# Optimization experiments

Hardware: AMD Instinct MI355X
Metric: run time of the kernel (lower is better)

Reference implementation:

```python
import jax, jax.numpy as jnp
import numpy as np


def setup_inputs() -> dict:
    key = jax.random.key(0)
    k1, k2, k3, k4 = jax.random.split(key, 4)
    dim, b, q_len, c_len = 1024, 16, 1024, 2048
    q = jax.random.normal(k1, (q_len, b, dim), dtype=jnp.float32)
    c = jax.random.normal(k2, (c_len, b, dim), dtype=jnp.float32)
    # torch nn.Linear weights: [out_features, in_features]
    W_in = jax.random.normal(k3, (dim, dim), dtype=jnp.float32) * (dim ** -0.5)
    W_out = jax.random.normal(k4, (dim, 2 * dim), dtype=jnp.float32) * ((2 * dim) ** -0.5)
    return {"q": q, "c": c, "W_in": W_in, "W_out": W_out}


def reference(q, c, W_in, W_out):
    # q: [q_len, b, dim] -> [b, q_len, dim]; c: [c_len, b, dim] -> [b, c_len, dim]
    qb = jnp.transpose(q, (1, 0, 2))
    cb = jnp.transpose(c, (1, 0, 2))
    qb = jnp.einsum('bqd,ed->bqe', qb, W_in)            # linear_in (no bias)
    score = jnp.einsum('bqd,bkd->bqk', qb, cb)          # unscaled QK^T
    score = jax.nn.softmax(score, axis=-1)              # [b, q_len, c_len]
    ctx = jnp.einsum('bqk,bkd->bqd', score, cb)         # score @ c
    cat = jnp.concatenate([ctx, qb], axis=-1)           # [b, q_len, 2*dim]
    out = jnp.tanh(jnp.einsum('bqf,df->bqd', cat, W_out))
    return (jnp.transpose(out, (1, 0, 2)), score)       # ([q_len,b,dim], [b,q_len,c_len])
```

## Files before the change

### kernel.cpp

```cpp
#include <hip/hip_runtime.h>
#include <hip/hip_bf16.h>
#include <stdint.h>


typedef __bf16 bf16x8 __attribute__((ext_vector_type(8)));
typedef float floatx4 __attribute__((ext_vector_type(4)));

__device__ __forceinline__ unsigned short f2bf_rne(float f) {
  unsigned int u = __float_as_uint(f);
  u += 0x7FFFu + ((u >> 16) & 1u);
  return (unsigned short)(u >> 16);
}
__device__ __forceinline__ float bf2f(unsigned short h) {
  return __uint_as_float(((unsigned int)h) << 16);
}

__device__ __forceinline__ void async_load16(const void* g, void* l) {
  __builtin_amdgcn_global_load_lds(
      (const __attribute__((address_space(1))) void*)g,
      (__attribute__((address_space(3))) void*)l,
      16, 0, 0);
}

__global__ __launch_bounds__(256) void split_kernel(
    const float* __restrict__ x, unsigned short* __restrict__ hi,
    unsigned short* __restrict__ lo, long n4)
{
  long i = (long)blockIdx.x * 256 + threadIdx.x;
  if (i >= n4) return;
  float4 v = ((const float4*)x)[i];
  ushort4 h;
  h.x = f2bf_rne(v.x); h.y = f2bf_rne(v.y);
  h.z = f2bf_rne(v.z); h.w = f2bf_rne(v.w);
  ((ushort4*)hi)[i] = h;
  if (lo) {
    ushort4 l;
    l.x = f2bf_rne(v.x - bf2f(h.x));
    l.y = f2bf_rne(v.y - bf2f(h.y));
    l.z = f2bf_rne(v.z - bf2f(h.z));
    l.w = f2bf_rne(v.w - bf2f(h.w));
    ((ushort4*)lo)[i] = l;
  }
}

__global__ __launch_bounds__(256) void transpose_kernel(
    const float* __restrict__ c, unsigned short* __restrict__ ct)
{
  __shared__ unsigned short t[64 * 68];
  int k0 = blockIdx.x * 64;
  int d0 = blockIdx.y * 64;
  int b  = blockIdx.z;
  int tid = threadIdx.x;
  #pragma unroll
  for (int p4 = 0; p4 < 4; ++p4) {
    int idx = p4 * 256 + tid;
    int kr = idx >> 4;
    int dc = (idx & 15) * 4;
    float4 v = *(const float4*)&c[(long)(k0 + kr) * 16384 + (long)b * 1024 + d0 + dc];
    ushort4 h;
    h.x = f2bf_rne(v.x); h.y = f2bf_rne(v.y);
    h.z = f2bf_rne(v.z); h.w = f2bf_rne(v.w);
    *(ushort4*)&t[kr * 68 + dc] = h;
  }
  __syncthreads();
  #pragma unroll
  for (int p4 = 0; p4 < 4; ++p4) {
    int idx = p4 * 256 + tid;
    int dr = idx >> 4;
    int kc = (idx & 15) * 4;
    ushort4 o;
    o.x = t[(kc + 0) * 68 + dr];
    o.y = t[(kc + 1) * 68 + dr];
    o.z = t[(kc + 2) * 68 + dr];
    o.w = t[(kc + 3) * 68 + dr];
    *(ushort4*)&ct[(long)b * 2097152 + (long)(d0 + dr) * 2048 + k0 + kc] = o;
  }
}

__global__ __launch_bounds__(256) void softmax_kernel(
    float* __restrict__ S, unsigned short* __restrict__ P)
{
  __shared__ float sred[8];
  long row = blockIdx.x;
  float* p = S + row * 2048;
  int tid = threadIdx.x;
  int lane = tid & 63, w = tid >> 6;
  float4 v0 = ((float4*)p)[tid];
  float4 v1 = ((float4*)p)[tid + 256];
  float m = fmaxf(fmaxf(fmaxf(v0.x, v0.y), fmaxf(v0.z, v0.w)),
                  fmaxf(fmaxf(v1.x, v1.y), fmaxf(v1.z, v1.w)));
  #pragma unroll
  for (int off = 32; off; off >>= 1) m = fmaxf(m, __shfl_xor(m, off));
  if (lane == 0) sred[w] = m;
  __syncthreads();
  m = fmaxf(fmaxf(sred[0], sred[1]), fmaxf(sred[2], sred[3]));
  v0.x = __expf(v0.x - m); v0.y = __expf(v0.y - m);
  v0.z = __expf(v0.z - m); v0.w = __expf(v0.w - m);
  v1.x = __expf(v1.x - m); v1.y = __expf(v1.y - m);
  v1.z = __expf(v1.z - m); v1.w = __expf(v1.w - m);
  float s = v0.x + v0.y + v0.z + v0.w + v1.x + v1.y + v1.z + v1.w;
  #pragma unroll
  for (int off = 32; off; off >>= 1) s += __shfl_xor(s, off);
  if (lane == 0) sred[4 + w] = s;
  __syncthreads();
  s = sred[4] + sred[5] + sred[6] + sred[7];
  float inv = 1.0f / s;
  v0.x *= inv; v0.y *= inv; v0.z *= inv; v0.w *= inv;
  v1.x *= inv; v1.y *= inv; v1.z *= inv; v1.w *= inv;
  ((float4*)p)[tid] = v0;
  ((float4*)p)[tid + 256] = v1;
  unsigned short* pp = P + row * 2048;
  ushort4 b0, b1;
  b0.x = f2bf_rne(v0.x); b0.y = f2bf_rne(v0.y);
  b0.z = f2bf_rne(v0.z); b0.w = f2bf_rne(v0.w);
  b1.x = f2bf_rne(v1.x); b1.y = f2bf_rne(v1.y);
  b1.z = f2bf_rne(v1.z); b1.w = f2bf_rne(v1.w);
  ((ushort4*)pp)[tid] = b0;
  ((ushort4*)pp)[tid + 256] = b1;
}

template<int SPLIT, int MODE>
__global__ __launch_bounds__(512, 2) void gemm_kernel(
    const unsigned short* __restrict__ Ah, const unsigned short* __restrict__ Al,
    long sAb, long ldA,
    const unsigned short* __restrict__ Bh, const unsigned short* __restrict__ Bl,
    long sBb, long ldB,
    void* __restrict__ Cp, long sCb, long ldC,
    unsigned short* __restrict__ P1, unsigned short* __restrict__ P2,
    int K, int SM, int SN, int GM)
{
  __shared__ __align__(16) unsigned short lds[65536];

  const int tid  = threadIdx.x;
  const int lane = tid & 63;
  const int w    = tid >> 6;
  const int wm   = w >> 2;
  const int wn   = w & 3;
  const int bz   = blockIdx.z;

  const int flat = blockIdx.x + gridDim.x * blockIdx.y;
  const int sub  = flat & 7;
  const int g    = flat >> 3;
  const long mt  = (long)(sub % GM) * SM + (g / SN);
  const long nt  = (long)(sub / GM) * SN + (g % SN);
  const long m0  = mt * 256;
  const long n0  = nt * 256;

  const unsigned short* a0 = Ah + bz * sAb + m0 * ldA;
  const unsigned short* a1 = SPLIT ? (Al + bz * sAb + m0 * ldA) : a0;
  const unsigned short* b0 = Bh + bz * sBb + n0 * ldB;
  const unsigned short* b1 = SPLIT ? (Bl + bz * sBb + n0 * ldB) : b0;

  const int s0r = tid >> 2,        s1r = (512 + tid) >> 2;
  const int s0k = (tid & 3) ^ ((s0r >> 1) & 3);
  const int s1k = ((512 + tid) & 3) ^ ((s1r >> 1) & 3);
  const long offA0 = (long)s0r * ldA + s0k * 8;
  const long offA1 = (long)s1r * ldA + s1k * 8;
  const long offB0 = (long)s0r * ldB + s0k * 8;
  const long offB1 = (long)s1r * ldB + s1k * 8;
  const int d0 = w * 512;
  const int d1 = 4096 + w * 512;

  const int nkt = SPLIT ? 3 * (K / 32) : (K / 32);

  floatx4 acc[8][4] = {};

  auto stage = [&](int vt2) {
    const int slot = vt2 & 3;
    const unsigned short* As;
    const unsigned short* Bs;
    long ks;
    if (SPLIT) {
      int term = vt2 % 3;
      ks = (long)(vt2 / 3) * 32;
      As = (term < 2) ? a0 : a1;
      Bs = (term == 1) ? b1 : b0;
    } else {
      As = a0; Bs = b0; ks = (long)vt2 * 32;
    }
    const int ab = slot * 8192;
    const int bb = 32768 + slot * 8192;
    async_load16(As + offA0 + ks, &lds[ab + d0]);
    async_load16(As + offA1 + ks, &lds[ab + d1]);
    async_load16(Bs + offB0 + ks, &lds[bb + d0]);
    async_load16(Bs + offB1 + ks, &lds[bb + d1]);
  };

  stage(0); stage(1); stage(2);

  for (int vt = 0; vt < nkt; ++vt) {
    const int ahead = nkt - 1 - vt;
    if (ahead >= 2)      asm volatile("s_waitcnt vmcnt(8)" ::: "memory");
    else if (ahead == 1) asm volatile("s_waitcnt vmcnt(4)" ::: "memory");
    else                 asm volatile("s_waitcnt vmcnt(0)" ::: "memory");
    __builtin_amdgcn_s_barrier();
    __builtin_amdgcn_sched_barrier(0);

    if (vt + 3 < nkt) stage(vt + 3);
    __builtin_amdgcn_sched_barrier(0);

    const unsigned short* At = &lds[(vt & 3) * 8192];
    const unsigned short* Bt = &lds[32768 + (vt & 3) * 8192];

    bf16x8 fb[4];
    #pragma unroll
    for (int j = 0; j < 4; ++j) {
      int r    = wn * 64 + j * 16 + (lane & 15);
      int slot = r * 4 + ((lane >> 4) ^ ((r >> 1) & 3));
      fb[j] = *(const bf16x8*)&Bt[slot * 8];
    }
    __builtin_amdgcn_s_setprio(1);
    #pragma unroll
    for (int i = 0; i < 8; ++i) {
      int r    = wm * 128 + i * 16 + (lane & 15);
      int slot = r * 4 + ((lane >> 4) ^ ((r >> 1) & 3));
      bf16x8 fa = *(const bf16x8*)&At[slot * 8];
      #pragma unroll
      for (int j = 0; j < 4; ++j)
        acc[i][j] = __builtin_amdgcn_mfma_f32_16x16x32_bf16(fa, fb[j], acc[i][j], 0, 0, 0);
    }
    __builtin_amdgcn_s_setprio(0);
  }

  #pragma unroll
  for (int i = 0; i < 8; ++i) {
    #pragma unroll
    for (int j = 0; j < 4; ++j) {
      #pragma unroll
      for (int t = 0; t < 4; ++t) {
        long rg = m0 + wm * 128 + i * 16 + (lane >> 4) * 4 + t;
        long cg = n0 + wn * 64 + j * 16 + (lane & 15);
        float v = acc[i][j][t];
        if (MODE == 0) {
          ((float*)Cp)[bz * sCb + rg * ldC + cg] = v;
        } else if (MODE == 1) {
          ((unsigned short*)Cp)[bz * sCb + rg * ldC + cg] = f2bf_rne(v);
        } else if (MODE == 2) {
          long qq = rg & 1023, bb = rg >> 10;
          ((float*)Cp)[(qq * 16 + bb) * 1024 + cg] = tanhf(v);
        } else {
          unsigned short hv = f2bf_rne(v);
          unsigned short lv = f2bf_rne(v - bf2f(hv));
          P1[rg * 1024 + cg] = hv;
          P2[rg * 1024 + cg] = lv;
          long bb = rg & 15, qq = rg >> 4;
          ((unsigned short*)Cp)[(bb * 1024 + qq) * 2048 + 1024 + cg] = hv;
        }
      }
    }
  }
}

extern "C" void kernel_launch(void* const* d_in, const int* in_sizes, int n_in,
                              void* d_out, int out_size, void* d_ws, size_t ws_size,
                              hipStream_t stream)
{
  const float* q    = (const float*)d_in[0];
  const float* c    = (const float*)d_in[1];
  const float* Win  = (const float*)d_in[2];
  const float* Wout = (const float*)d_in[3];

  char* ws = (char*)d_ws;
  const size_t MB = 1024u * 1024u;

  unsigned short* qh  = (unsigned short*)(ws);
  unsigned short* ch  = (unsigned short*)(ws);
  unsigned short* pb  = (unsigned short*)(ws);
  unsigned short* qbh = (unsigned short*)(ws + 64 * MB);
  unsigned short* qbl = (unsigned short*)(ws + 96 * MB);
  unsigned short* ct  = (unsigned short*)(ws + 64 * MB);
  unsigned short* cat = (unsigned short*)(ws + 128 * MB);
  unsigned short* Wh  = (unsigned short*)(ws + 192 * MB);
  unsigned short* Wl  = (unsigned short*)(ws + 194 * MB);
  unsigned short* Wo  = (unsigned short*)(ws + 196 * MB);

  unsigned short* ql  = (unsigned short*)d_out;
  unsigned short* cl  = (unsigned short*)d_out;
  float* out0  = (float*)d_out;
  float* score = (float*)d_out + 16777216;

  split_kernel<<<16384, 256, 0, stream>>>(q,    qh, ql,      4194304L);
  split_kernel<<<1024,  256, 0, stream>>>(Win,  Wh, Wl,      262144L);
  split_kernel<<<2048,  256, 0, stream>>>(Wout, Wo, nullptr, 524288L);

  gemm_kernel<1, 3><<<dim3(32, 8, 1), 512, 0, stream>>>(
      qh, ql, 0L, 1024L, Wh, Wl, 0L, 1024L,
      (void*)cat, 0L, 0L, qbh, qbl, 1024, 8, 4, 8);

  split_kernel<<<32768, 256, 0, stream>>>(c, ch, cl, 8388608L);

  gemm_kernel<1, 0><<<dim3(4, 8, 16), 512, 0, stream>>>(
      qbh, qbl, 1024L, 16384L, ch, cl, 1024L, 16384L,
      (void*)score, 2097152L, 2048L, nullptr, nullptr, 1024, 2, 2, 2);

  transpose_kernel<<<dim3(32, 16, 16), 256, 0, stream>>>(c, ct);
  softmax_kernel<<<16384, 256, 0, stream>>>(score, pb);

  gemm_kernel<0, 1><<<dim3(4, 4, 16), 512, 0, stream>>>(
      pb, nullptr, 2097152L, 2048L, ct, nullptr, 2097152L, 2048L,
      (void*)cat, 2097152L, 2048L, nullptr, nullptr, 2048, 1, 2, 4);

  gemm_kernel<0, 2><<<dim3(32, 8, 1), 512, 0, stream>>>(
      cat, nullptr, 0L, 2048L, Wo, nullptr, 0L, 2048L,
      (void*)out0, 0L, 0L, nullptr, nullptr, 2048, 8, 4, 8);

  (void)in_sizes; (void)n_in; (void)out_size; (void)ws_size;
}
```

Baseline: 929.3 us.

## Stage hi and lo split tiles once per k-step in split-bf16 GEMM

In the split-bf16 (three-term) GEMM path, each k-slice's hi and lo tiles of A and B are now loaded once into LDS and reused across the three hi*hi, hi*lo and lo*hi MFMA passes. Previously each term re-staged its own A/B pair, which loaded hi tiles twice. This cuts global-to-LDS traffic by about a third. The pipeline depth becomes one k-step ahead with two barriers per step, which may expose more load latency than the earlier three-stage prefetch.

```diff
diff --git a/kernel.cpp b/kernel.cpp
--- a/kernel.cpp
+++ b/kernel.cpp
@@ -161,65 +161,140 @@
   const int d0 = w * 512;
   const int d1 = 4096 + w * 512;
 
-  const int nkt = SPLIT ? 3 * (K / 32) : (K / 32);
-
   floatx4 acc[8][4] = {};
 
-  auto stage = [&](int vt2) {
-    const int slot = vt2 & 3;
-    const unsigned short* As;
-    const unsigned short* Bs;
-    long ks;
-    if (SPLIT) {
-      int term = vt2 % 3;
-      ks = (long)(vt2 / 3) * 32;
-      As = (term < 2) ? a0 : a1;
-      Bs = (term == 1) ? b1 : b0;
-    } else {
-      As = a0; Bs = b0; ks = (long)vt2 * 32;
+  if constexpr (SPLIT) {
+    const int nk = K / 32;
+
+    auto stageE = [&](int k, int h) {
+      const int slot = (2 * k + h) & 3;
+      const unsigned short* As = h ? a1 : a0;
+      const unsigned short* Bs = h ? b1 : b0;
+      const long ks = (long)k * 32;
+      const int ab = slot * 8192;
+      const int bb = 32768 + slot * 8192;
+      async_load16(As + offA0 + ks, &lds[ab + d0]);
+      async_load16(As + offA1 + ks, &lds[ab + d1]);
+      async_load16(Bs + offB0 + ks, &lds[bb + d0]);
+      async_load16(Bs + offB1 + ks, &lds[bb + d1]);
+    };
+
+    stageE(0, 0); stageE(0, 1);
+
+    for (int k = 0; k < nk; ++k) {
+      asm volatile("s_waitcnt vmcnt(4)" ::: "memory");
+      __builtin_amdgcn_s_barrier();
+      __builtin_amdgcn_sched_barrier(0);
+
+      if (k + 1 < nk) { stageE(k + 1, 0); stageE(k + 1, 1); }
+      __builtin_amdgcn_sched_barrier(0);
+
+      const unsigned short* Ah_t = &lds[((2 * k) & 3) * 8192];
+      const unsigned short* Bh_t = &lds[32768 + ((2 * k) & 3) * 8192];
+      const unsigned short* Al_t = &lds[((2 * k + 1) & 3) * 8192];
+      const unsigned short* Bl_t = &lds[32768 + ((2 * k + 1) & 3) * 8192];
+
+      bf16x8 fbh[4];
+      #pragma unroll
+      for (int j = 0; j < 4; ++j) {
+        int r    = wn * 64 + j * 16 + (lane & 15);
+        int slot = r * 4 + ((lane >> 4) ^ ((r >> 1) & 3));
+        fbh[j] = *(const bf16x8*)&Bh_t[slot * 8];
+      }
+      __builtin_amdgcn_s_setprio(1);
+      #pragma unroll
+      for (int i = 0; i < 8; ++i) {
+        int r    = wm * 128 + i * 16 + (lane & 15);
+        int slot = r * 4 + ((lane >> 4) ^ ((r >> 1) & 3));
+        bf16x8 fah = *(const bf16x8*)&Ah_t[slot * 8];
+        #pragma unroll
+        for (int j = 0; j < 4; ++j)
+          acc[i][j] = __builtin_amdgcn_mfma_f32_16x16x32_bf16(fah, fbh[j], acc[i][j], 0, 0, 0);
+      }
+      __builtin_amdgcn_s_setprio(0);
+
+      if (k + 1 < nk) asm volatile("s_waitcnt vmcnt(8)" ::: "memory");
+      else            asm volatile("s_waitcnt vmcnt(0)" ::: "memory");
+      __builtin_amdgcn_s_barrier();
+      __builtin_amdgcn_sched_barrier(0);
+
+      bf16x8 fbl[4];
+      #pragma unroll
+      for (int j = 0; j < 4; ++j) {
+        int r    = wn * 64 + j * 16 + (lane & 15);
+        int slot = r * 4 + ((lane >> 4) ^ ((r >> 1) & 3));
+        fbl[j] = *(const bf16x8*)&Bl_t[slot * 8];
+      }
+      __builtin_amdgcn_s_setprio(1);
+      #pragma unroll
+      for (int i = 0; i < 8; ++i) {
+        int r    = wm * 128 + i * 16 + (lane & 15);
+        int slot = r * 4 + ((lane >> 4) ^ ((r >> 1) & 3));
+        bf16x8 fah = *(const bf16x8*)&Ah_t[slot * 8];
+        #pragma unroll
+        for (int j = 0; j < 4; ++j)
+          acc[i][j] = __builtin_amdgcn_mfma_f32_16x16x32_bf16(fah, fbl[j], acc[i][j], 0, 0, 0);
+      }
+      #pragma unroll
+      for (int i = 0; i < 8; ++i) {
+        int r    = wm * 128 + i * 16 + (lane & 15);
+        int slot = r * 4 + ((lane >> 4) ^ ((r >> 1) & 3));
+        bf16x8 fal = *(const bf16x8*)&Al_t[slot * 8];
+        #pragma unroll
+        for (int j = 0; j < 4; ++j)
+          acc[i][j] = __builtin_amdgcn_mfma_f32_16x16x32_bf16(fal, fbh[j], acc[i][j], 0, 0, 0);
+      }
+      __builtin_amdgcn_s_setprio(0);
     }
-    const int ab = slot * 8192;
-    const int bb = 32768 + slot * 8192;
-    async_load16(As + offA0 + ks, &lds[ab + d0]);
-    async_load16(As + offA1 + ks, &lds[ab + d1]);
-    async_load16(Bs + offB0 + ks, &lds[bb + d0]);
-    async_load16(Bs + offB1 + ks, &lds[bb + d1]);
-  };
-
-  stage(0); stage(1); stage(2);
-
-  for (int vt = 0; vt < nkt; ++vt) {
-    const int ahead = nkt - 1 - vt;
-    if (ahead >= 2)      asm volatile("s_waitcnt vmcnt(8)" ::: "memory");
-    else if (ahead == 1) asm volatile("s_waitcnt vmcnt(4)" ::: "memory");
-    else                 asm volatile("s_waitcnt vmcnt(0)" ::: "memory");
-    __builtin_amdgcn_s_barrier();
-    __builtin_amdgcn_sched_barrier(0);
-
-    if (vt + 3 < nkt) stage(vt + 3);
-    __builtin_amdgcn_sched_barrier(0);
-
-    const unsigned short* At = &lds[(vt & 3) * 8192];
-    const unsigned short* Bt = &lds[32768 + (vt & 3) * 8192];
-
-    bf16x8 fb[4];
-    #pragma unroll
-    for (int j = 0; j < 4; ++j) {
-      int r    = wn * 64 + j * 16 + (lane & 15);
-      int slot = r * 4 + ((lane >> 4) ^ ((r >> 1) & 3));
-      fb[j] = *(const bf16x8*)&Bt[slot * 8];
+  } else {
+    const int nkt = K / 32;
+
+    auto stage = [&](int vt2) {
+      const int slot = vt2 & 3;
+      const long ks = (long)vt2 * 32;
+      const int ab = slot * 8192;
+      const int bb = 32768 + slot * 8192;
+      async_load16(a0 + offA0 + ks, &lds[ab + d0]);
+      async_load16(a0 + offA1 + ks, &lds[ab + d1]);
+      async_load16(b0 + offB0 + ks, &lds[bb + d0]);
+      async_load16(b0 + offB1 + ks, &lds[bb + d1]);
+    };
+
+    stage(0); stage(1); stage(2);
+
+    for (int vt = 0; vt < nkt; ++vt) {
+      const int ahead = nkt - 1 - vt;
+      if (ahead >= 2)      asm volatile("s_waitcnt vmcnt(8)" ::: "memory");
+      else if (ahead == 1) asm volatile("s_waitcnt vmcnt(4)" ::: "memory");
+      else                 asm volatile("s_waitcnt vmcnt(0)" ::: "memory");
+      __builtin_amdgcn_s_barrier();
+      __builtin_amdgcn_sched_barrier(0);
+
+      if (vt + 3 < nkt) stage(vt + 3);
+      __builtin_amdgcn_sched_barrier(0);
+
+      const unsigned short* At = &lds[(vt & 3) * 8192];
+      const unsigned short* Bt = &lds[32768 + (vt & 3) * 8192];
+
+      bf16x8 fb[4];
+      #pragma unroll
+      for (int j = 0; j < 4; ++j) {
+        int r    = wn * 64 + j * 16 + (lane & 15);
+        int slot = r * 4 + ((lane >> 4) ^ ((r >> 1) & 3));
+        fb[j] = *(const bf16x8*)&Bt[slot * 8];
+      }
+      __builtin_amdgcn_s_setprio(1);
+      #pragma unroll
+      for (int i = 0; i < 8; ++i) {
+        int r    = wm * 128 + i * 16 + (lane & 15);
+        int slot = r * 4 + ((lane >> 4) ^ ((r >> 1) & 3));
+        bf16x8 fa = *(const bf16x8*)&At[slot * 8];
+        #pragma unroll
+        for (int j = 0; j < 4; ++j)
+          acc[i][j] = __builtin_amdgcn_mfma_f32_16x16x32_bf16(fa, fb[j], acc[i][j], 0, 0, 0);
+      }
+      __builtin_amdgcn_s_setprio(0);
     }
-    __builtin_amdgcn_s_setprio(1);
-    #pragma unroll
-    for (int i = 0; i < 8; ++i) {
-      int r    = wm * 128 + i * 16 + (lane & 15);
-      int slot = r * 4 + ((lane >> 4) ^ ((r >> 1) & 3));
-      bf16x8 fa = *(const bf16x8*)&At[slot * 8];
-      #pragma unroll
-      for (int j = 0; j < 4; ++j)
-        acc[i][j] = __builtin_amdgcn_mfma_f32_16x16x32_bf16(fa, fb[j], acc[i][j], 0, 0, 0);
-    }
-    __builtin_amdgcn_s_setprio(0);
   }
 
   #pragma unroll
```

New measurement: 908.4 us. 1.02x faster.
